# Optimization experiments

Measured on AMD Instinct MI355X. Metric: run time of the kernel, lower is better.

Reference implementation:

```python
import jax, jax.numpy as jnp
import numpy as np

D_MODEL = 1024
NUM_HEADS = 16
D_K = D_MODEL // NUM_HEADS
B, L = 2, 2048


def setup_inputs() -> dict:
    key = jax.random.key(0)
    ks = jax.random.split(key, 10)
    s = 1.0 / np.sqrt(D_MODEL)
    inp = {
        "x": jax.random.normal(ks[0], (B, L, D_MODEL), dtype=jnp.float32),
        "mask": jnp.ones((B, L, L), dtype=jnp.int32),
        "wq": jax.random.uniform(ks[1], (D_MODEL, D_MODEL), jnp.float32, -s, s),
        "bq": jax.random.uniform(ks[2], (D_MODEL,), jnp.float32, -s, s),
        "wk": jax.random.uniform(ks[3], (D_MODEL, D_MODEL), jnp.float32, -s, s),
        "bk": jax.random.uniform(ks[4], (D_MODEL,), jnp.float32, -s, s),
        "wv": jax.random.uniform(ks[5], (D_MODEL, D_MODEL), jnp.float32, -s, s),
        "bv": jax.random.uniform(ks[6], (D_MODEL,), jnp.float32, -s, s),
        "wo": jax.random.uniform(ks[7], (D_MODEL, D_MODEL), jnp.float32, -s, s),
        "bo": jax.random.uniform(ks[8], (D_MODEL,), jnp.float32, -s, s),
    }
    return inp


def reference(x, mask, wq, bq, wk, bk, wv, bv, wo, bo):
    Bs, Ls, C = x.shape
    # linear projections, then split heads: [B, L, C] -> [B, h, L, d_k]
    def split_heads(t):
        return t.reshape(Bs, Ls, NUM_HEADS, D_K).transpose(0, 2, 1, 3)
    q = split_heads(x @ wq + bq)
    k = split_heads(x @ wk + bk)
    v = split_heads(x @ wv + bv)
    scores = jnp.einsum("bhlc,bhkc->bhlk", q, k) / np.sqrt(D_K)
    # mask: [B, L, L] -> [B, 1, L, L]; fill masked positions with -1e9
    scores = jnp.where(mask[:, None, :, :] == 0, jnp.float32(-1e9), scores)
    attn = jax.nn.softmax(scores, axis=-1)  # dropout p=0.0 -> identity
    out = jnp.einsum("bhlk,bhkc->bhlc", attn, v)
    out = out.transpose(0, 2, 1, 3).reshape(Bs, Ls, C)
    return out @ wo + bo
```

## Files before the change

### kernel.cpp

```cpp
#include <hip/hip_runtime.h>
#include <stdint.h>

#define D_MODEL 1024
#define NHEAD   16
#define DK      64
#define BATCH   2
#define SEQ     2048
#define MTOT    (BATCH*SEQ)

typedef unsigned short u16;
typedef unsigned int   u32;
typedef u16    u16x4  __attribute__((ext_vector_type(4)));
typedef u16    u16x8  __attribute__((ext_vector_type(8)));
typedef u32    u32x4  __attribute__((ext_vector_type(4)));
typedef __bf16 bf16x8 __attribute__((ext_vector_type(8)));
typedef float  f32x4  __attribute__((ext_vector_type(4)));
typedef float  f32x16 __attribute__((ext_vector_type(16)));

__device__ __forceinline__ u16 f2bf(float f) {
  union { float f; unsigned u; } v; v.f = f;
  return (u16)((v.u + 0x7fffu + ((v.u >> 16) & 1u)) >> 16);
}

__device__ __forceinline__ void gl_lds16(const void* g, void* l) {
  __builtin_amdgcn_global_load_lds((const __attribute__((address_space(1))) void*)g,
                                   (__attribute__((address_space(3))) void*)l, 16, 0, 0);
}

__device__ __forceinline__ bf16x8 ld_frag(const u16* p) {
  return __builtin_bit_cast(bf16x8, *(const u16x8*)p);
}

__device__ __forceinline__ u32 cvtpk(float lo, float hi) {
  u32 r;
  asm("v_cvt_pk_bf16_f32 %0, %1, %2" : "=v"(r) : "v"(lo), "v"(hi));
  return r;
}

__global__ __launch_bounds__(256) void k_cvt_x(const float* __restrict__ x, u16* __restrict__ xb) {
  int i = blockIdx.x * 256 + threadIdx.x;
  const float4 v = ((const float4*)x)[i];
  u16x4 o; o[0]=f2bf(v.x); o[1]=f2bf(v.y); o[2]=f2bf(v.z); o[3]=f2bf(v.w);
  *(u16x4*)(xb + (size_t)i*4) = o;
}

__global__ __launch_bounds__(256) void k_wtrans(const float* __restrict__ wq, const float* __restrict__ wk,
                                                const float* __restrict__ wv, const float* __restrict__ wo,
                                                u16* __restrict__ wqkv_t, u16* __restrict__ wo_t) {
  __shared__ float tile[32][33];
  const int z = blockIdx.z;
  const float* src = (z==0)?wq:(z==1)?wk:(z==2)?wv:wo;
  const int kb = blockIdx.y*32, nb = blockIdx.x*32;
  const int tx = threadIdx.x & 31, ty = threadIdx.x >> 5;
  #pragma unroll
  for (int i=0;i<4;i++)
    tile[ty + i*8][tx] = src[(size_t)(kb + ty + i*8)*D_MODEL + nb + tx];
  __syncthreads();
  u16* dst = (z<3) ? (wqkv_t + (size_t)z*D_MODEL*D_MODEL) : wo_t;
  #pragma unroll
  for (int i=0;i<4;i++) {
    int n = nb + ty + i*8, k = kb + tx;
    dst[(size_t)n*D_MODEL + k] = f2bf(tile[tx][ty + i*8]);
  }
}

__global__ __launch_bounds__(256) void k_maskpack(const int* __restrict__ mask,
                                                  unsigned long long* __restrict__ mb) {
  const int wid = blockIdx.x*4 + (threadIdx.x >> 6);
  const int lane = threadIdx.x & 63;
  for (int t2 = 0; t2 < 32; ++t2) {
    int word = wid*32 + t2;
    int row = word >> 5;
    int kb = word & 31;
    int m = mask[(size_t)row*SEQ + kb*64 + lane];
    unsigned long long bits = __ballot(m != 0);
    if (lane == 0) mb[word] = bits;
  }
}

__global__ __launch_bounds__(256) void k_vtrans(const u16* __restrict__ V, u16* __restrict__ Vt) {
  __shared__ u16 tile[64][72];
  const int bh = blockIdx.x >> 5;
  const int l0 = (blockIdx.x & 31) * 64;
  const int t = threadIdx.x;
  const u16* src = V + ((size_t)bh*SEQ + l0)*DK;
  #pragma unroll
  for (int j=0;j<2;j++) {
    int idx = t + j*256;
    int r = idx >> 3, c8 = (idx & 7)*8;
    *(u16x8*)&tile[r][c8] = *(const u16x8*)(src + (size_t)r*DK + c8);
  }
  __syncthreads();
  u16* dst = Vt + (size_t)bh*DK*SEQ + l0;
  #pragma unroll
  for (int j=0;j<2;j++) {
    int idx = t + j*256;
    int d = idx >> 3, k8 = (idx & 7)*8;
    u16x8 o;
    #pragma unroll
    for (int e=0;e<8;e++) o[e] = tile[k8 + e][d];
    *(u16x8*)(dst + (size_t)d*SEQ + k8) = o;
  }
}

template<int EPI>
__global__ __launch_bounds__(256) void k_gemm(const u16* __restrict__ A, const u16* __restrict__ Bt,
                                              const int M, const int N, const int K, const int nbm,
                                              const float* __restrict__ bq, const float* __restrict__ bk,
                                              const float* __restrict__ bv,
                                              u16* __restrict__ Qo, u16* __restrict__ Ko, u16* __restrict__ Vo,
                                              const float* __restrict__ bo, float* __restrict__ out) {
  __shared__ u16 As[128*32];
  __shared__ u16 Bs[128*32];
  const int t = threadIdx.x, lane = t & 63, w = t >> 6;
  const int bm = blockIdx.x % nbm, bn = blockIdx.x / nbm;
  const int brow = bm*128, bcol = bn*128;

  const int srow = w*32 + (lane >> 2);
  const int sswz = (lane & 3) ^ ((lane >> 2) & 3);
  const u16* aS0 = A  + (size_t)(brow + srow)*K + sswz*8;
  const u16* aS1 = aS0 + (size_t)16*K;
  const u16* bS0 = Bt + (size_t)(bcol + srow)*K + sswz*8;
  const u16* bS1 = bS0 + (size_t)16*K;
  u16* aD0 = As + w*1024; u16* aD1 = aD0 + 512;
  u16* bD0 = Bs + w*1024; u16* bD1 = bD0 + 512;

  const int wr = w >> 1, wc = w & 1;
  const int slotA = (lane >> 4) ^ (lane & 3);
  const u16* aRd = As + (wr*64 + (lane & 15))*32 + slotA*8;
  const u16* bRd = Bs + (wc*64 + (lane & 15))*32 + slotA*8;

  f32x4 acc[4][4];
  #pragma unroll
  for (int i=0;i<4;i++)
    #pragma unroll
    for (int j=0;j<4;j++) acc[i][j] = (f32x4){0.f,0.f,0.f,0.f};

  for (int kt = 0; kt < K; kt += 32) {
    gl_lds16(aS0 + kt, aD0);
    gl_lds16(aS1 + kt, aD1);
    gl_lds16(bS0 + kt, bD0);
    gl_lds16(bS1 + kt, bD1);
    __syncthreads();
    bf16x8 af[4], bfr[4];
    #pragma unroll
    for (int m=0;m<4;m++) af[m] = ld_frag(aRd + m*512);
    #pragma unroll
    for (int n=0;n<4;n++) bfr[n] = ld_frag(bRd + n*512);
    #pragma unroll
    for (int m=0;m<4;m++)
      #pragma unroll
      for (int n=0;n<4;n++)
        acc[m][n] = __builtin_amdgcn_mfma_f32_16x16x32_bf16(af[m], bfr[n], acc[m][n], 0,0,0);
    __syncthreads();
  }

  const int orow = brow + wr*64 + (lane >> 4)*4;
  const int ocol = bcol + wc*64 + (lane & 15);
  if (EPI == 0) {
    const int mat = ocol >> 10;
    const float* bias = (mat==0) ? bq : (mat==1) ? bk : bv;
    u16* outp = (mat==0) ? Qo : (mat==1) ? Ko : Vo;
    const float scal = (mat==0) ? 0.125f*1.4426950408889634f : 1.0f;
    #pragma unroll
    for (int m=0;m<4;m++) {
      #pragma unroll
      for (int n=0;n<4;n++) {
        int col = ocol + n*16;
        int c = col & 1023;
        float bb = bias[c];
        int h = c >> 6, d = c & 63;
        #pragma unroll
        for (int j=0;j<4;j++) {
          int row = orow + m*16 + j;
          int b = row >> 11, l = row & 2047;
          float v = (acc[m][n][j] + bb) * scal;
          outp[(((size_t)(b*NHEAD + h)*SEQ + l) << 6) + d] = f2bf(v);
        }
      }
    }
  } else {
    #pragma unroll
    for (int m=0;m<4;m++)
      #pragma unroll
      for (int n=0;n<4;n++) {
        int col = ocol + n*16;
        float bb = bo[col];
        #pragma unroll
        for (int j=0;j<4;j++) {
          int row = orow + m*16 + j;
          out[(size_t)row*N + col] = acc[m][n][j] + bb;
        }
      }
  }
}

__global__ __launch_bounds__(256) void k_attn(const u16* __restrict__ Q, const u16* __restrict__ K,
                                              const u16* __restrict__ Vt,
                                              const unsigned long long* __restrict__ MB,
                                              u16* __restrict__ AO) {
  __shared__ u16 Ks[64*64];
  __shared__ u16 Vs[64*64];
  const int t = threadIdx.x, lane = t & 63, w = t >> 6;
  const int bh = blockIdx.x >> 4;
  const int q0 = (blockIdx.x & 15) * 128;
  const int b = bh >> 4, h = bh & 15;
  const int lq = lane & 31, hi = lane >> 5, l7 = lane & 7;

  const int qg = q0 + w*32 + lq;
  const u16* qp = Q + ((size_t)bh*SEQ + qg)*DK + hi*8;
  bf16x8 qf[4];
  #pragma unroll
  for (int ks=0;ks<4;ks++) qf[ks] = ld_frag(qp + ks*16);

  const int srow = w*16 + (lane >> 3);
  const int sswz = l7 ^ ((lane >> 3) & 7);
  const u16* kS0 = K  + ((size_t)bh*SEQ + srow)*DK + sswz*8;
  const u16* kS1 = kS0 + 8*DK;
  const u16* vS0 = Vt + ((size_t)bh*DK + srow)*SEQ + sswz*8;
  const u16* vS1 = vS0 + 8*SEQ;
  u16* kD0 = Ks + w*1024; u16* kD1 = kD0 + 512;
  u16* vD0 = Vs + w*1024; u16* vD1 = vD0 + 512;

  f32x16 o0 = 0.f, o1 = 0.f;
  float m_run = -1e30f, l_run = 0.f;
  const unsigned long long* mbp = MB + ((size_t)b*SEQ + qg)*32;

  for (int kt = 0; kt < SEQ/64; ++kt) {
    gl_lds16(kS0, kD0); gl_lds16(kS1, kD1);
    gl_lds16(vS0, vD0); gl_lds16(vS1, vD1);
    kS0 += 64*DK; kS1 += 64*DK; vS0 += 64; vS1 += 64;
    __syncthreads();

    f32x16 s0 = 0.f, s1 = 0.f;
    #pragma unroll
    for (int ks=0;ks<4;ks++) {
      const int ph = (ks*2 + hi) ^ l7;
      bf16x8 kf0 = ld_frag(Ks + lq*64 + ph*8);
      bf16x8 kf1 = ld_frag(Ks + (32+lq)*64 + ph*8);
      s0 = __builtin_amdgcn_mfma_f32_32x32x16_bf16(kf0, qf[ks], s0, 0,0,0);
      s1 = __builtin_amdgcn_mfma_f32_32x32x16_bf16(kf1, qf[ks], s1, 0,0,0);
    }

    unsigned long long mb = mbp[kt];
    if (!__all(mb == ~0ull)) {
      #pragma unroll
      for (int r=0;r<16;r++) {
        int kl = (r&3) + 8*(r>>2) + 4*hi;
        if (!((mb >> kl) & 1ull)) s0[r] = -1e9f;
        if (!((mb >> (kl+32)) & 1ull)) s1[r] = -1e9f;
      }
    }

    float mx = -1e30f;
    #pragma unroll
    for (int r=0;r<16;r++) { mx = fmaxf(mx, s0[r]); mx = fmaxf(mx, s1[r]); }
    mx = fmaxf(mx, __shfl_xor(mx, 32));
    float m_new = fmaxf(m_run, mx);
    float corr = __builtin_amdgcn_exp2f(m_run - m_new);
    float ps = 0.f;
    #pragma unroll
    for (int r=0;r<16;r++) {
      s0[r] = __builtin_amdgcn_exp2f(s0[r] - m_new); ps += s0[r];
      s1[r] = __builtin_amdgcn_exp2f(s1[r] - m_new); ps += s1[r];
    }
    ps += __shfl_xor(ps, 32);
    l_run = l_run * corr + ps;
    m_run = m_new;
    #pragma unroll
    for (int r=0;r<16;r++) { o0[r] *= corr; o1[r] *= corr; }

    #pragma unroll
    for (int kt2=0;kt2<2;kt2++) {
      const f32x16& sv = kt2 ? s1 : s0;
      u32 w0 = cvtpk(sv[0],  sv[1]),  w1 = cvtpk(sv[2],  sv[3]);
      u32 w2 = cvtpk(sv[4],  sv[5]),  w3 = cvtpk(sv[6],  sv[7]);
      u32 w4 = cvtpk(sv[8],  sv[9]),  w5 = cvtpk(sv[10], sv[11]);
      u32 w6 = cvtpk(sv[12], sv[13]), w7 = cvtpk(sv[14], sv[15]);
      asm volatile("v_permlane32_swap_b32 %0, %1" : "+v"(w0), "+v"(w2));
      asm volatile("v_permlane32_swap_b32 %0, %1" : "+v"(w1), "+v"(w3));
      asm volatile("v_permlane32_swap_b32 %0, %1" : "+v"(w4), "+v"(w6));
      asm volatile("v_permlane32_swap_b32 %0, %1" : "+v"(w5), "+v"(w7));
      bf16x8 pa0 = __builtin_bit_cast(bf16x8, (u32x4){w0, w1, w2, w3});
      bf16x8 pa1 = __builtin_bit_cast(bf16x8, (u32x4){w4, w5, w6, w7});
      const int ph0 = ((kt2*2+0)*2 + hi) ^ l7;
      const int ph1 = ((kt2*2+1)*2 + hi) ^ l7;
      bf16x8 v00 = ld_frag(Vs + lq*64      + ph0*8);
      bf16x8 v01 = ld_frag(Vs + lq*64      + ph1*8);
      bf16x8 v10 = ld_frag(Vs + (32+lq)*64 + ph0*8);
      bf16x8 v11 = ld_frag(Vs + (32+lq)*64 + ph1*8);
      o0 = __builtin_amdgcn_mfma_f32_32x32x16_bf16(v00, pa0, o0, 0,0,0);
      o0 = __builtin_amdgcn_mfma_f32_32x32x16_bf16(v01, pa1, o0, 0,0,0);
      o1 = __builtin_amdgcn_mfma_f32_32x32x16_bf16(v10, pa0, o1, 0,0,0);
      o1 = __builtin_amdgcn_mfma_f32_32x32x16_bf16(v11, pa1, o1, 0,0,0);
    }
    __syncthreads();
  }

  const float inv = 1.0f / l_run;
  size_t base = ((size_t)(b*SEQ + qg))*D_MODEL + h*DK;
  #pragma unroll
  for (int rr=0;rr<4;rr++) {
    u16x4 g0, g1;
    #pragma unroll
    for (int i=0;i<4;i++) { g0[i] = f2bf(o0[rr*4+i]*inv); g1[i] = f2bf(o1[rr*4+i]*inv); }
    *(u16x4*)(AO + base + rr*8 + hi*4)      = g0;
    *(u16x4*)(AO + base + 32 + rr*8 + hi*4) = g1;
  }
}

extern "C" void kernel_launch(void* const* d_in, const int* in_sizes, int n_in,
                              void* d_out, int out_size, void* d_ws, size_t ws_size,
                              hipStream_t stream) {
  const float* x  = (const float*)d_in[0];
  const int*  msk = (const int*)d_in[1];
  const float* wq = (const float*)d_in[2];
  const float* bq = (const float*)d_in[3];
  const float* wk = (const float*)d_in[4];
  const float* bk = (const float*)d_in[5];
  const float* wv = (const float*)d_in[6];
  const float* bv = (const float*)d_in[7];
  const float* wo = (const float*)d_in[8];
  const float* bo = (const float*)d_in[9];
  float* out = (float*)d_out;

  char* ws = (char*)d_ws;
  size_t off = 0;
  u16* Xb   = (u16*)(ws + off); off += (size_t)MTOT*D_MODEL*2;
  u16* Wqkv = (u16*)(ws + off); off += (size_t)3*D_MODEL*D_MODEL*2;
  u16* Wot  = (u16*)(ws + off); off += (size_t)D_MODEL*D_MODEL*2;
  u16* Qb   = (u16*)(ws + off); off += (size_t)BATCH*NHEAD*SEQ*DK*2;
  u16* Kb   = (u16*)(ws + off); off += (size_t)BATCH*NHEAD*SEQ*DK*2;
  u16* Vb   = (u16*)(ws + off); off += (size_t)BATCH*NHEAD*SEQ*DK*2;
  u16* Vtb  = (u16*)(ws + off); off += (size_t)BATCH*NHEAD*SEQ*DK*2;
  u16* AO   = (u16*)(ws + off); off += (size_t)MTOT*D_MODEL*2;
  unsigned long long* Mb = (unsigned long long*)(ws + off);

  k_cvt_x<<<MTOT*D_MODEL/4/256, 256, 0, stream>>>(x, Xb);
  k_wtrans<<<dim3(32,32,4), 256, 0, stream>>>(wq, wk, wv, wo, Wqkv, Wot);
  k_maskpack<<<1024, 256, 0, stream>>>(msk, Mb);
  k_gemm<0><<<(MTOT/128)*(3*D_MODEL/128), 256, 0, stream>>>(
      Xb, Wqkv, MTOT, 3*D_MODEL, D_MODEL, MTOT/128,
      bq, bk, bv, Qb, Kb, Vb, nullptr, nullptr);
  k_vtrans<<<BATCH*NHEAD*(SEQ/64), 256, 0, stream>>>(Vb, Vtb);
  k_attn<<<BATCH*NHEAD*(SEQ/128), 256, 0, stream>>>(Qb, Kb, Vtb, Mb, AO);
  k_gemm<1><<<(MTOT/128)*(D_MODEL/128), 256, 0, stream>>>(
      AO, Wot, MTOT, D_MODEL, D_MODEL, MTOT/128,
      nullptr, nullptr, nullptr, nullptr, nullptr, nullptr, bo, out);
}
```

Before: 154.1 us.

## Double-buffer K/V tiles, lazy rescale, MFMA row-sum, block swizzle in attention

The attention kernel now double-buffers K and V tiles in shared memory, so the next tile's global-to-LDS load is issued before the current tile is computed, and it drops one barrier per iteration. It also skips the output rescale unless the running max grows by more than a threshold. The softmax denominator is computed with extra MFMAs against a ones vector instead of shuffle reductions, and the block index is swizzled and s_setprio is set around the MFMA sections. The aim is to hide load latency and cut VALU and shuffle work, at the cost of twice the LDS, two extra MFMAs per step, and a lazy-rescale threshold that depends on score magnitudes.

```diff
diff --git a/kernel.cpp b/kernel.cpp
--- a/kernel.cpp
+++ b/kernel.cpp
@@ -199,11 +199,13 @@
                                               const u16* __restrict__ Vt,
                                               const unsigned long long* __restrict__ MB,
                                               u16* __restrict__ AO) {
-  __shared__ u16 Ks[64*64];
-  __shared__ u16 Vs[64*64];
+  __shared__ u16 Ks[2][64*64];
+  __shared__ u16 Vs[2][64*64];
   const int t = threadIdx.x, lane = t & 63, w = t >> 6;
-  const int bh = blockIdx.x >> 4;
-  const int q0 = (blockIdx.x & 15) * 128;
+  const int bid = blockIdx.x;
+  const int swz = (bid & 7)*64 + (bid >> 3);
+  const int bh = swz >> 4;
+  const int q0 = (swz & 15) * 128;
   const int b = bh >> 4, h = bh & 15;
   const int lq = lane & 31, hi = lane >> 5, l7 = lane & 7;
 
@@ -215,32 +217,47 @@
 
   const int srow = w*16 + (lane >> 3);
   const int sswz = l7 ^ ((lane >> 3) & 7);
-  const u16* kS0 = K  + ((size_t)bh*SEQ + srow)*DK + sswz*8;
-  const u16* kS1 = kS0 + 8*DK;
-  const u16* vS0 = Vt + ((size_t)bh*DK + srow)*SEQ + sswz*8;
-  const u16* vS1 = vS0 + 8*SEQ;
-  u16* kD0 = Ks + w*1024; u16* kD1 = kD0 + 512;
-  u16* vD0 = Vs + w*1024; u16* vD1 = vD0 + 512;
-
-  f32x16 o0 = 0.f, o1 = 0.f;
-  float m_run = -1e30f, l_run = 0.f;
+  const u16* kSb = K  + ((size_t)bh*SEQ + srow)*DK + sswz*8;
+  const u16* vSb = Vt + ((size_t)bh*DK + srow)*SEQ + sswz*8;
+
+  u16x8 ones8;
+  #pragma unroll
+  for (int i=0;i<8;i++) ones8[i] = 0x3F80;
+  const bf16x8 ones = __builtin_bit_cast(bf16x8, ones8);
+
+  f32x16 o0 = 0.f, o1 = 0.f, lacc = 0.f;
+  float m_run = -1e30f;
   const unsigned long long* mbp = MB + ((size_t)b*SEQ + qg)*32;
 
-  for (int kt = 0; kt < SEQ/64; ++kt) {
-    gl_lds16(kS0, kD0); gl_lds16(kS1, kD1);
-    gl_lds16(vS0, vD0); gl_lds16(vS1, vD1);
-    kS0 += 64*DK; kS1 += 64*DK; vS0 += 64; vS1 += 64;
-    __syncthreads();
+  #define NT (SEQ/64)
+  #define STAGE(buf, tile) do {                                   \
+    const u16* kp_ = kSb + (size_t)(tile)*64*DK;                  \
+    const u16* vp_ = vSb + (tile)*64;                             \
+    u16* kd_ = &Ks[buf][w*1024];                                  \
+    u16* vd_ = &Vs[buf][w*1024];                                  \
+    gl_lds16(kp_, kd_); gl_lds16(kp_ + 8*DK, kd_ + 512);          \
+    gl_lds16(vp_, vd_); gl_lds16(vp_ + 8*SEQ, vd_ + 512);         \
+  } while (0)
+
+  STAGE(0, 0);
+  asm volatile("s_waitcnt vmcnt(0)" ::: "memory");
+  __builtin_amdgcn_s_barrier();
+
+  for (int kt = 0; kt < NT; ++kt) {
+    const int cur = kt & 1;
+    if (kt + 1 < NT) STAGE(cur ^ 1, kt + 1);
 
     f32x16 s0 = 0.f, s1 = 0.f;
+    __builtin_amdgcn_s_setprio(1);
     #pragma unroll
     for (int ks=0;ks<4;ks++) {
       const int ph = (ks*2 + hi) ^ l7;
-      bf16x8 kf0 = ld_frag(Ks + lq*64 + ph*8);
-      bf16x8 kf1 = ld_frag(Ks + (32+lq)*64 + ph*8);
+      bf16x8 kf0 = ld_frag(&Ks[cur][lq*64 + ph*8]);
+      bf16x8 kf1 = ld_frag(&Ks[cur][(32+lq)*64 + ph*8]);
       s0 = __builtin_amdgcn_mfma_f32_32x32x16_bf16(kf0, qf[ks], s0, 0,0,0);
       s1 = __builtin_amdgcn_mfma_f32_32x32x16_bf16(kf1, qf[ks], s1, 0,0,0);
     }
+    __builtin_amdgcn_s_setprio(0);
 
     unsigned long long mb = mbp[kt];
     if (!__all(mb == ~0ull)) {
@@ -254,21 +271,21 @@
 
     float mx = -1e30f;
     #pragma unroll
-    for (int r=0;r<16;r++) { mx = fmaxf(mx, s0[r]); mx = fmaxf(mx, s1[r]); }
+    for (int r=0;r<16;r++) mx = fmaxf(fmaxf(mx, s0[r]), s1[r]);
     mx = fmaxf(mx, __shfl_xor(mx, 32));
-    float m_new = fmaxf(m_run, mx);
-    float corr = __builtin_amdgcn_exp2f(m_run - m_new);
-    float ps = 0.f;
+    if (!__all(mx <= m_run + 8.0f)) {
+      float m_new = fmaxf(m_run, mx);
+      float corr = __builtin_amdgcn_exp2f(m_run - m_new);
+      lacc[0] *= corr;
+      #pragma unroll
+      for (int r=0;r<16;r++) { o0[r] *= corr; o1[r] *= corr; }
+      m_run = m_new;
+    }
     #pragma unroll
     for (int r=0;r<16;r++) {
-      s0[r] = __builtin_amdgcn_exp2f(s0[r] - m_new); ps += s0[r];
-      s1[r] = __builtin_amdgcn_exp2f(s1[r] - m_new); ps += s1[r];
-    }
-    ps += __shfl_xor(ps, 32);
-    l_run = l_run * corr + ps;
-    m_run = m_new;
-    #pragma unroll
-    for (int r=0;r<16;r++) { o0[r] *= corr; o1[r] *= corr; }
+      s0[r] = __builtin_amdgcn_exp2f(s0[r] - m_run);
+      s1[r] = __builtin_amdgcn_exp2f(s1[r] - m_run);
+    }
 
     #pragma unroll
     for (int kt2=0;kt2<2;kt2++) {
@@ -285,19 +302,26 @@
       bf16x8 pa1 = __builtin_bit_cast(bf16x8, (u32x4){w4, w5, w6, w7});
       const int ph0 = ((kt2*2+0)*2 + hi) ^ l7;
       const int ph1 = ((kt2*2+1)*2 + hi) ^ l7;
-      bf16x8 v00 = ld_frag(Vs + lq*64      + ph0*8);
-      bf16x8 v01 = ld_frag(Vs + lq*64      + ph1*8);
-      bf16x8 v10 = ld_frag(Vs + (32+lq)*64 + ph0*8);
-      bf16x8 v11 = ld_frag(Vs + (32+lq)*64 + ph1*8);
+      bf16x8 v00 = ld_frag(&Vs[cur][lq*64      + ph0*8]);
+      bf16x8 v01 = ld_frag(&Vs[cur][lq*64      + ph1*8]);
+      bf16x8 v10 = ld_frag(&Vs[cur][(32+lq)*64 + ph0*8]);
+      bf16x8 v11 = ld_frag(&Vs[cur][(32+lq)*64 + ph1*8]);
+      __builtin_amdgcn_s_setprio(1);
       o0 = __builtin_amdgcn_mfma_f32_32x32x16_bf16(v00, pa0, o0, 0,0,0);
       o0 = __builtin_amdgcn_mfma_f32_32x32x16_bf16(v01, pa1, o0, 0,0,0);
       o1 = __builtin_amdgcn_mfma_f32_32x32x16_bf16(v10, pa0, o1, 0,0,0);
       o1 = __builtin_amdgcn_mfma_f32_32x32x16_bf16(v11, pa1, o1, 0,0,0);
-    }
-    __syncthreads();
-  }
-
-  const float inv = 1.0f / l_run;
+      lacc = __builtin_amdgcn_mfma_f32_32x32x16_bf16(ones, pa0, lacc, 0,0,0);
+      lacc = __builtin_amdgcn_mfma_f32_32x32x16_bf16(ones, pa1, lacc, 0,0,0);
+      __builtin_amdgcn_s_setprio(0);
+    }
+
+    asm volatile("s_waitcnt vmcnt(0)" ::: "memory");
+    __builtin_amdgcn_s_barrier();
+  }
+  #undef STAGE
+
+  const float inv = 1.0f / lacc[0];
   size_t base = ((size_t)(b*SEQ + qg))*D_MODEL + h*DK;
   #pragma unroll
   for (int rr=0;rr<4;rr++) {
```

After: 199.5 us. 29.5% more time.

## Split attention KV range across two wave groups, merge partial softmax states

Applied to the files above, without the earlier changes.

The attention kernel now launches 512 threads per block, with two groups of four waves each handling half of the key sequence (split-K flash attention). The partial outputs, running max and sum are merged through shared memory at the end. It also adds lazy rescaling, which skips the correction unless the max grows by more than a threshold, tree reductions for max and sum, and block-index swizzling for cache locality. This raises parallelism per block and shortens the serial loop, at the cost of more LDS, an extra merge step and higher register pressure under the launch bounds.

```diff
diff --git a/kernel.cpp b/kernel.cpp
--- a/kernel.cpp
+++ b/kernel.cpp
@@ -195,54 +195,59 @@
   }
 }
 
-__global__ __launch_bounds__(256) void k_attn(const u16* __restrict__ Q, const u16* __restrict__ K,
-                                              const u16* __restrict__ Vt,
-                                              const unsigned long long* __restrict__ MB,
-                                              u16* __restrict__ AO) {
-  __shared__ u16 Ks[64*64];
-  __shared__ u16 Vs[64*64];
+__global__ __launch_bounds__(512, 4) void k_attn(const u16* __restrict__ Q, const u16* __restrict__ K,
+                                                 const u16* __restrict__ Vt,
+                                                 const unsigned long long* __restrict__ MB,
+                                                 u16* __restrict__ AO) {
+  __shared__ char smem[36864];
   const int t = threadIdx.x, lane = t & 63, w = t >> 6;
-  const int bh = blockIdx.x >> 4;
-  const int q0 = (blockIdx.x & 15) * 128;
+  const int hf = w >> 2, widx = w & 3;
+  const int bid = blockIdx.x;
+  const int swz = (bid & 7)*64 + (bid >> 3);
+  const int bh = swz >> 4;
+  const int q0 = (swz & 15) * 128;
   const int b = bh >> 4, h = bh & 15;
   const int lq = lane & 31, hi = lane >> 5, l7 = lane & 7;
 
-  const int qg = q0 + w*32 + lq;
+  u16* Kbuf = (u16*)(smem + hf*16384);
+  u16* Vbuf = (u16*)(smem + hf*16384 + 8192);
+
+  const int qg = q0 + widx*32 + lq;
   const u16* qp = Q + ((size_t)bh*SEQ + qg)*DK + hi*8;
   bf16x8 qf[4];
   #pragma unroll
   for (int ks=0;ks<4;ks++) qf[ks] = ld_frag(qp + ks*16);
 
-  const int srow = w*16 + (lane >> 3);
+  const int srow = widx*16 + (lane >> 3);
   const int sswz = l7 ^ ((lane >> 3) & 7);
-  const u16* kS0 = K  + ((size_t)bh*SEQ + srow)*DK + sswz*8;
-  const u16* kS1 = kS0 + 8*DK;
-  const u16* vS0 = Vt + ((size_t)bh*DK + srow)*SEQ + sswz*8;
-  const u16* vS1 = vS0 + 8*SEQ;
-  u16* kD0 = Ks + w*1024; u16* kD1 = kD0 + 512;
-  u16* vD0 = Vs + w*1024; u16* vD1 = vD0 + 512;
+  const u16* kSb = K  + ((size_t)bh*SEQ + srow)*DK + sswz*8;
+  const u16* vSb = Vt + ((size_t)bh*DK + srow)*SEQ + sswz*8;
+  u16* kD0 = Kbuf + widx*1024; u16* kD1 = kD0 + 512;
+  u16* vD0 = Vbuf + widx*1024; u16* vD1 = vD0 + 512;
 
   f32x16 o0 = 0.f, o1 = 0.f;
   float m_run = -1e30f, l_run = 0.f;
   const unsigned long long* mbp = MB + ((size_t)b*SEQ + qg)*32;
 
-  for (int kt = 0; kt < SEQ/64; ++kt) {
-    gl_lds16(kS0, kD0); gl_lds16(kS1, kD1);
-    gl_lds16(vS0, vD0); gl_lds16(vS1, vD1);
-    kS0 += 64*DK; kS1 += 64*DK; vS0 += 64; vS1 += 64;
+  for (int i = 0; i < 16; ++i) {
+    const int ktg = hf*16 + i;
+    const u16* kp = kSb + (size_t)ktg*64*DK;
+    const u16* vp = vSb + ktg*64;
+    gl_lds16(kp, kD0); gl_lds16(kp + 8*DK, kD1);
+    gl_lds16(vp, vD0); gl_lds16(vp + 8*SEQ, vD1);
     __syncthreads();
 
     f32x16 s0 = 0.f, s1 = 0.f;
     #pragma unroll
     for (int ks=0;ks<4;ks++) {
       const int ph = (ks*2 + hi) ^ l7;
-      bf16x8 kf0 = ld_frag(Ks + lq*64 + ph*8);
-      bf16x8 kf1 = ld_frag(Ks + (32+lq)*64 + ph*8);
+      bf16x8 kf0 = ld_frag(Kbuf + lq*64 + ph*8);
+      bf16x8 kf1 = ld_frag(Kbuf + (32+lq)*64 + ph*8);
       s0 = __builtin_amdgcn_mfma_f32_32x32x16_bf16(kf0, qf[ks], s0, 0,0,0);
       s1 = __builtin_amdgcn_mfma_f32_32x32x16_bf16(kf1, qf[ks], s1, 0,0,0);
     }
 
-    unsigned long long mb = mbp[kt];
+    unsigned long long mb = mbp[ktg];
     if (!__all(mb == ~0ull)) {
       #pragma unroll
       for (int r=0;r<16;r++) {
@@ -252,23 +257,34 @@
       }
     }
 
-    float mx = -1e30f;
-    #pragma unroll
-    for (int r=0;r<16;r++) { mx = fmaxf(mx, s0[r]); mx = fmaxf(mx, s1[r]); }
-    mx = fmaxf(mx, __shfl_xor(mx, 32));
-    float m_new = fmaxf(m_run, mx);
-    float corr = __builtin_amdgcn_exp2f(m_run - m_new);
-    float ps = 0.f;
+    float tm[16];
+    #pragma unroll
+    for (int r=0;r<16;r++) tm[r] = fmaxf(s0[r], s1[r]);
+    #pragma unroll
+    for (int st=8; st>0; st>>=1)
+      #pragma unroll
+      for (int r=0;r<8;r++) if (r < st) tm[r] = fmaxf(tm[r], tm[r+st]);
+    float mx = fmaxf(tm[0], __shfl_xor(tm[0], 32));
+    if (!__all(mx <= m_run + 8.0f)) {
+      float m_new = fmaxf(m_run, mx);
+      float corr = __builtin_amdgcn_exp2f(m_run - m_new);
+      l_run *= corr;
+      #pragma unroll
+      for (int r=0;r<16;r++) { o0[r] *= corr; o1[r] *= corr; }
+      m_run = m_new;
+    }
+    float ts[16];
     #pragma unroll
     for (int r=0;r<16;r++) {
-      s0[r] = __builtin_amdgcn_exp2f(s0[r] - m_new); ps += s0[r];
-      s1[r] = __builtin_amdgcn_exp2f(s1[r] - m_new); ps += s1[r];
-    }
-    ps += __shfl_xor(ps, 32);
-    l_run = l_run * corr + ps;
-    m_run = m_new;
-    #pragma unroll
-    for (int r=0;r<16;r++) { o0[r] *= corr; o1[r] *= corr; }
+      s0[r] = __builtin_amdgcn_exp2f(s0[r] - m_run);
+      s1[r] = __builtin_amdgcn_exp2f(s1[r] - m_run);
+      ts[r] = s0[r] + s1[r];
+    }
+    #pragma unroll
+    for (int st=8; st>0; st>>=1)
+      #pragma unroll
+      for (int r=0;r<8;r++) if (r < st) ts[r] += ts[r+st];
+    l_run += ts[0] + __shfl_xor(ts[0], 32);
 
     #pragma unroll
     for (int kt2=0;kt2<2;kt2++) {
@@ -285,10 +301,10 @@
       bf16x8 pa1 = __builtin_bit_cast(bf16x8, (u32x4){w4, w5, w6, w7});
       const int ph0 = ((kt2*2+0)*2 + hi) ^ l7;
       const int ph1 = ((kt2*2+1)*2 + hi) ^ l7;
-      bf16x8 v00 = ld_frag(Vs + lq*64      + ph0*8);
-      bf16x8 v01 = ld_frag(Vs + lq*64      + ph1*8);
-      bf16x8 v10 = ld_frag(Vs + (32+lq)*64 + ph0*8);
-      bf16x8 v11 = ld_frag(Vs + (32+lq)*64 + ph1*8);
+      bf16x8 v00 = ld_frag(Vbuf + lq*64      + ph0*8);
+      bf16x8 v01 = ld_frag(Vbuf + lq*64      + ph1*8);
+      bf16x8 v10 = ld_frag(Vbuf + (32+lq)*64 + ph0*8);
+      bf16x8 v11 = ld_frag(Vbuf + (32+lq)*64 + ph1*8);
       o0 = __builtin_amdgcn_mfma_f32_32x32x16_bf16(v00, pa0, o0, 0,0,0);
       o0 = __builtin_amdgcn_mfma_f32_32x32x16_bf16(v01, pa1, o0, 0,0,0);
       o1 = __builtin_amdgcn_mfma_f32_32x32x16_bf16(v10, pa0, o1, 0,0,0);
@@ -297,15 +313,35 @@
     __syncthreads();
   }
 
-  const float inv = 1.0f / l_run;
-  size_t base = ((size_t)(b*SEQ + qg))*D_MODEL + h*DK;
-  #pragma unroll
-  for (int rr=0;rr<4;rr++) {
-    u16x4 g0, g1;
-    #pragma unroll
-    for (int i=0;i<4;i++) { g0[i] = f2bf(o0[rr*4+i]*inv); g1[i] = f2bf(o1[rr*4+i]*inv); }
-    *(u16x4*)(AO + base + rr*8 + hi*4)      = g0;
-    *(u16x4*)(AO + base + 32 + rr*8 + hi*4) = g1;
+  float* marea = (float*)smem;
+  if (hf == 1) {
+    float* p = marea + (size_t)(widx*64 + lane)*35;
+    #pragma unroll
+    for (int r=0;r<16;r++) { p[r] = o0[r]; p[16+r] = o1[r]; }
+    p[32] = m_run; p[33] = l_run;
+  }
+  __syncthreads();
+  if (hf == 0) {
+    const float* p = marea + (size_t)(widx*64 + lane)*35;
+    float m1 = p[32], l1 = p[33];
+    float mm = fmaxf(m_run, m1);
+    float c0 = __builtin_amdgcn_exp2f(m_run - mm);
+    float c1 = __builtin_amdgcn_exp2f(m1 - mm);
+    float inv = 1.0f / (l_run*c0 + l1*c1);
+    size_t base = ((size_t)(b*SEQ + qg))*D_MODEL + h*DK;
+    u16x4 g;
+    #pragma unroll
+    for (int rr=0;rr<4;rr++) {
+      #pragma unroll
+      for (int i2=0;i2<4;i2++) g[i2] = f2bf((o0[rr*4+i2]*c0 + p[rr*4+i2]*c1) * inv);
+      *(u16x4*)(AO + base + rr*8 + hi*4) = g;
+    }
+    #pragma unroll
+    for (int rr=0;rr<4;rr++) {
+      #pragma unroll
+      for (int i2=0;i2<4;i2++) g[i2] = f2bf((o1[rr*4+i2]*c0 + p[16+rr*4+i2]*c1) * inv);
+      *(u16x4*)(AO + base + 32 + rr*8 + hi*4) = g;
+    }
   }
 }
 
@@ -343,7 +379,7 @@
       Xb, Wqkv, MTOT, 3*D_MODEL, D_MODEL, MTOT/128,
       bq, bk, bv, Qb, Kb, Vb, nullptr, nullptr);
   k_vtrans<<<BATCH*NHEAD*(SEQ/64), 256, 0, stream>>>(Vb, Vtb);
-  k_attn<<<BATCH*NHEAD*(SEQ/128), 256, 0, stream>>>(Qb, Kb, Vtb, Mb, AO);
+  k_attn<<<BATCH*NHEAD*(SEQ/128), 512, 0, stream>>>(Qb, Kb, Vtb, Mb, AO);
   k_gemm<1><<<(MTOT/128)*(D_MODEL/128), 256, 0, stream>>>(
       AO, Wot, MTOT, D_MODEL, D_MODEL, MTOT/128,
       nullptr, nullptr, nullptr, nullptr, nullptr, nullptr, bo, out);
```

After: 151.7 us. About the same (-1.6%).
